# Kernel optimization log

Measured on AMD Instinct MI355X. Metric: run time of the kernel, lower is better.

## Reference

```python
import jax, jax.numpy as jnp
import numpy as np

B, S, HID, NH = 2, 2048, 2048, 16
HD = HID // NH  # head_dim = 128


def setup_inputs() -> dict:
    key = jax.random.key(0)
    ks = jax.random.split(key, 10)
    sc = 1.0 / np.sqrt(HID)
    inp = {
        "hidden_state": jax.random.normal(ks[0], (B, S, HID), dtype=jnp.float32),
        # upper-triangular (strict) causal mask: 1 where attention is forbidden
        "casual_mask": jnp.triu(jnp.ones((S, S), dtype=jnp.float32), k=1),
        # pad last 128 tokens of each sequence
        "pad_mask": jnp.concatenate(
            [jnp.zeros((B, S - 128), jnp.float32), jnp.ones((B, 128), jnp.float32)], axis=1
        ),
        # weights stored [in, out] (transposed vs torch Linear)
        "Wq": jax.random.normal(ks[1], (HID, HID), dtype=jnp.float32) * sc,
        "bq": jnp.zeros((HID,), jnp.float32),
        "Wk": jax.random.normal(ks[2], (HID, HD), dtype=jnp.float32) * sc,
        "bk": jnp.zeros((HD,), jnp.float32),
        "Wv": jax.random.normal(ks[3], (HID, HD), dtype=jnp.float32) * sc,
        "bv": jnp.zeros((HD,), jnp.float32),
        "Wo": jax.random.normal(ks[4], (HID, HID), dtype=jnp.float32) * sc,
        "bo": jnp.zeros((HID,), jnp.float32),
    }
    return inp


def reference(hidden_state, casual_mask, pad_mask, Wq, bq, Wk, bk, Wv, bv, Wo, bo):
    bsz, seq_len, hid = hidden_state.shape
    nh = NH
    hd = hid // nh
    q = hidden_state @ Wq + bq                      # [B,S,HID]
    k = hidden_state @ Wk + bk                      # [B,S,HD]  single shared head
    v = hidden_state @ Wv + bv                      # [B,S,HD]
    q = q.reshape(bsz, seq_len, nh, hd).transpose(0, 2, 1, 3)  # [B,NH,S,HD]
    # attn scores: shared K broadcast across all query heads
    scores = jnp.einsum("bhqd,bkd->bhqk", q, k) / jnp.sqrt(jnp.float32(hd))
    scores = scores + casual_mask * (-1e9)
    scores = scores + pad_mask[:, None, None, :] * (-1e9)
    probs = jax.nn.softmax(scores, axis=-1)         # [B,NH,S,S]
    out = jnp.einsum("bhqk,bkd->bhqd", probs, v)    # [B,NH,S,HD]
    out = out.transpose(0, 2, 1, 3).reshape(bsz, seq_len, hid)
    return out @ Wo + bo
```

## Files before the change

### kernel.cpp

```cpp
#include <hip/hip_runtime.h>
#include <hip/hip_bf16.h>
#include <math.h>

#define B_    2
#define S_    2048
#define HID_  2048
#define NH_   16
#define HD_   128
#define MTOT  4096
#define QKV_N 2304

typedef short bf16x8 __attribute__((ext_vector_type(8)));
typedef float f32x4  __attribute__((ext_vector_type(4)));
typedef float f32x16 __attribute__((ext_vector_type(16)));

__device__ __forceinline__ ushort f2bf(float f) {
    __hip_bfloat16 h = __float2bfloat16(f);
    ushort u; __builtin_memcpy(&u, &h, 2); return u;
}

__device__ __forceinline__ void gload_lds16(const void* g, void* l) {
    __builtin_amdgcn_global_load_lds(
        (const __attribute__((address_space(1))) void*)g,
        (__attribute__((address_space(3))) void*)l, 16, 0, 0);
}
__device__ __forceinline__ void gload_lds4(const void* g, void* l) {
    __builtin_amdgcn_global_load_lds(
        (const __attribute__((address_space(1))) void*)g,
        (__attribute__((address_space(3))) void*)l, 4, 0, 0);
}

__global__ void cast_f32_bf16(const float* __restrict__ in, ushort* __restrict__ out)
{
    long i = ((long)blockIdx.x * 256 + threadIdx.x) * 8;
    float4 a = *(const float4*)&in[i];
    float4 b = *(const float4*)&in[i + 4];
    uint4 o;
    o.x = (uint)f2bf(a.x) | ((uint)f2bf(a.y) << 16);
    o.y = (uint)f2bf(a.z) | ((uint)f2bf(a.w) << 16);
    o.z = (uint)f2bf(b.x) | ((uint)f2bf(b.y) << 16);
    o.w = (uint)f2bf(b.z) | ((uint)f2bf(b.w) << 16);
    *(uint4*)&out[i] = o;
}

__global__ void transcast(const float* __restrict__ W, ushort* __restrict__ T,
                          int N, int rowoff)
{
    __shared__ float tile[32][33];
    const int tx = threadIdx.x & 31, ty = threadIdx.x >> 5;
    const int n0 = blockIdx.x * 32, k0 = blockIdx.y * 32;
#pragma unroll
    for (int i = 0; i < 4; i++)
        tile[ty + 8 * i][tx] = W[(long)(k0 + ty + 8 * i) * N + n0 + tx];
    __syncthreads();
#pragma unroll
    for (int i = 0; i < 4; i++)
        T[(long)(rowoff + n0 + ty + 8 * i) * 2048 + k0 + tx] = f2bf(tile[tx][ty + 8 * i]);
}

__global__ void fuse_bias(const float* __restrict__ bq, const float* __restrict__ bk,
                          const float* __restrict__ bv, float* __restrict__ bqkv)
{
    int i = blockIdx.x * 256 + threadIdx.x;
    if (i < 2048)      bqkv[i] = bq[i];
    else if (i < 2176) bqkv[i] = bk[i - 2048];
    else if (i < QKV_N) bqkv[i] = bv[i - 2176];
}

__global__ __launch_bounds__(256, 2) void gemm_qkv(
    const ushort* __restrict__ A, const ushort* __restrict__ Bt,
    const float* __restrict__ bias,
    ushort* __restrict__ qbuf, ushort* __restrict__ kbuf,
    ushort* __restrict__ vtbuf)
{
    const int K = HID_;
    __shared__ __align__(16) ushort As[128 * 32];
    __shared__ __align__(16) ushort Bs[128 * 32];
    const int t = threadIdx.x;
    const int w = t >> 6, l = t & 63;
    const long bm = (long)blockIdx.y * 128;
    const long bn = (long)blockIdx.x * 128;

    f32x4 acc[4][4];
#pragma unroll
    for (int i = 0; i < 4; i++)
#pragma unroll
        for (int j = 0; j < 4; j++) acc[i][j] = (f32x4){0.f, 0.f, 0.f, 0.f};

    const int srow = w * 16 + (l >> 2);
    const int scol = (l & 3) * 8;
    const ushort* Ag0 = A + (bm + srow) * (long)K + scol;
    const ushort* Ag1 = A + (bm + srow + 64) * (long)K + scol;
    const ushort* Bg0 = Bt + (bn + srow) * (long)K + scol;
    const ushort* Bg1 = Bt + (bn + srow + 64) * (long)K + scol;
    ushort* Al0 = As + w * 512;
    ushort* Al1 = As + 2048 + w * 512;
    ushort* Bl0 = Bs + w * 512;
    ushort* Bl1 = Bs + 2048 + w * 512;

    const int mrow = l & 15, kq = l >> 4;
    const int moff = (w & 1) * 64, noff = (w >> 1) * 64;

    for (int k0 = 0; k0 < K; k0 += 32) {
        gload_lds16(Ag0 + k0, Al0);
        gload_lds16(Ag1 + k0, Al1);
        gload_lds16(Bg0 + k0, Bl0);
        gload_lds16(Bg1 + k0, Bl1);
        __syncthreads();
        bf16x8 af[4], bfr[4];
#pragma unroll
        for (int i = 0; i < 4; i++)
            af[i] = *(const bf16x8*)&As[(moff + i * 16 + mrow) * 32 + kq * 8];
#pragma unroll
        for (int j = 0; j < 4; j++)
            bfr[j] = *(const bf16x8*)&Bs[(noff + j * 16 + mrow) * 32 + kq * 8];
#pragma unroll
        for (int i = 0; i < 4; i++)
#pragma unroll
            for (int j = 0; j < 4; j++)
                acc[i][j] = __builtin_amdgcn_mfma_f32_16x16x32_bf16(
                    af[i], bfr[j], acc[i][j], 0, 0, 0);
        __syncthreads();
    }

    const int crow = (l >> 4) * 4, ccol = l & 15;
    const int tile = blockIdx.x;
#pragma unroll
    for (int i = 0; i < 4; i++) {
#pragma unroll
        for (int j = 0; j < 4; j++) {
            long colg = bn + noff + j * 16 + ccol;
            float bv = bias[colg];
            long row0 = bm + moff + i * 16 + crow;
            float v[4];
#pragma unroll
            for (int r = 0; r < 4; r++) v[r] = acc[i][j][r] + bv;
            if (tile < 16) {
#pragma unroll
                for (int r = 0; r < 4; r++)
                    qbuf[(row0 + r) * (long)HID_ + colg] = f2bf(v[r]);
            } else if (tile == 16) {
                long ck = colg - 2048;
#pragma unroll
                for (int r = 0; r < 4; r++)
                    kbuf[(row0 + r) * (long)HD_ + ck] = f2bf(v[r]);
            } else {
                long cv = colg - 2176;
                long b  = row0 >> 11;
                long s0 = row0 & 2047;
                ushort4 pk;
                pk.x = f2bf(v[0]); pk.y = f2bf(v[1]);
                pk.z = f2bf(v[2]); pk.w = f2bf(v[3]);
                *(ushort4*)&vtbuf[b * (HD_ * (long)S_) + cv * (long)S_ + s0] = pk;
            }
        }
    }
}

__global__ __launch_bounds__(256, 2) void gemm_mfma(
    const ushort* __restrict__ A, const ushort* __restrict__ Bt,
    const float* __restrict__ bias, float* __restrict__ C,
    int K, int ldc)
{
    __shared__ __align__(16) ushort As[128 * 32];
    __shared__ __align__(16) ushort Bs[128 * 32];
    const int t = threadIdx.x;
    const int w = t >> 6, l = t & 63;
    const long bm = (long)blockIdx.y * 128;
    const long bn = (long)blockIdx.x * 128;

    f32x4 acc[4][4];
#pragma unroll
    for (int i = 0; i < 4; i++)
#pragma unroll
        for (int j = 0; j < 4; j++) acc[i][j] = (f32x4){0.f, 0.f, 0.f, 0.f};

    const int srow = w * 16 + (l >> 2);
    const int scol = (l & 3) * 8;
    const ushort* Ag0 = A + (bm + srow) * (long)K + scol;
    const ushort* Ag1 = A + (bm + srow + 64) * (long)K + scol;
    const ushort* Bg0 = Bt + (bn + srow) * (long)K + scol;
    const ushort* Bg1 = Bt + (bn + srow + 64) * (long)K + scol;
    ushort* Al0 = As + w * 512;
    ushort* Al1 = As + 2048 + w * 512;
    ushort* Bl0 = Bs + w * 512;
    ushort* Bl1 = Bs + 2048 + w * 512;

    const int mrow = l & 15, kq = l >> 4;
    const int moff = (w & 1) * 64, noff = (w >> 1) * 64;

    for (int k0 = 0; k0 < K; k0 += 32) {
        gload_lds16(Ag0 + k0, Al0);
        gload_lds16(Ag1 + k0, Al1);
        gload_lds16(Bg0 + k0, Bl0);
        gload_lds16(Bg1 + k0, Bl1);
        __syncthreads();
        bf16x8 af[4], bfr[4];
#pragma unroll
        for (int i = 0; i < 4; i++)
            af[i] = *(const bf16x8*)&As[(moff + i * 16 + mrow) * 32 + kq * 8];
#pragma unroll
        for (int j = 0; j < 4; j++)
            bfr[j] = *(const bf16x8*)&Bs[(noff + j * 16 + mrow) * 32 + kq * 8];
#pragma unroll
        for (int i = 0; i < 4; i++)
#pragma unroll
            for (int j = 0; j < 4; j++)
                acc[i][j] = __builtin_amdgcn_mfma_f32_16x16x32_bf16(
                    af[i], bfr[j], acc[i][j], 0, 0, 0);
        __syncthreads();
    }

    const int crow = (l >> 4) * 4, ccol = l & 15;
#pragma unroll
    for (int i = 0; i < 4; i++) {
#pragma unroll
        for (int j = 0; j < 4; j++) {
            long col = bn + noff + j * 16 + ccol;
            float bv = bias[col];
#pragma unroll
            for (int r = 0; r < 4; r++) {
                long row = bm + moff + i * 16 + crow + r;
                C[row * (long)ldc + col] = acc[i][j][r] + bv;
            }
        }
    }
}

__global__ __launch_bounds__(256, 2) void attn_mfma(
    const ushort* __restrict__ qbuf, const ushort* __restrict__ kbuf,
    const ushort* __restrict__ vtbuf, const float* __restrict__ pad,
    ushort* __restrict__ outp)
{
    __shared__ __align__(16) char smem[34816];
    ushort* Ks   = (ushort*)smem;
    ushort* Vt   = (ushort*)(smem + 16384);
    float*  padL = (float*)(smem + 32768);

    const int qblk = 15 - (int)blockIdx.x;
    const int h = blockIdx.y, b = blockIdx.z;
    const int t = threadIdx.x, w = t >> 6, l = t & 63;
    const int l31 = l & 31, h5 = l >> 5;
    const long rowbase = (long)b * S_;
    const int qbase = qblk * 128 + w * 32;

    bf16x8 qf[8];
    {
        const ushort* qp = qbuf + (rowbase + qbase + l31) * (long)HID_
                                + h * HD_ + h5 * 8;
#pragma unroll
        for (int ks = 0; ks < 8; ks++) qf[ks] = *(const bf16x8*)(qp + ks * 16);
    }

    f32x16 o[4] = {};
    float mrun = -1e30f, lrun = 0.f;

    const ushort* kg[4]; ushort* kl[4];
    const ushort* vg[4]; ushort* vl[4];
#pragma unroll
    for (int i = 0; i < 4; i++) {
        int key0 = w * 16 + i * 4 + (l >> 4);
        int gk = (l & 15) ^ (key0 & 15);
        kg[i] = kbuf + (rowbase + key0) * (long)HD_ + gk * 8;
        kl[i] = Ks + (w * 16 + i * 4) * 128 + l * 8;
        int d = w * 32 + i * 8 + (l >> 3);
        int gv = (l & 7) ^ (d & 7);
        vg[i] = vtbuf + ((long)b * HD_ + d) * (long)S_ + gv * 8;
        vl[i] = Vt + (w * 32 + i * 8) * 64 + l * 8;
    }

    const int kTiles = 2 * qblk + 2;
    const int qmaxw = qbase + 31;
    const float SC  = 0.08838834764831845f * 1.44269504089f;
    const float NEG = -1.0e9f * 1.44269504089f;

    for (int kt = 0; kt < kTiles; kt++) {
        const int ktb = kt * 64;
#pragma unroll
        for (int i = 0; i < 4; i++) gload_lds16(kg[i] + (long)ktb * HD_, kl[i]);
#pragma unroll
        for (int i = 0; i < 4; i++) gload_lds16(vg[i] + ktb, vl[i]);
        if (w == 0) gload_lds4(pad + rowbase + ktb + l, padL);
        __syncthreads();

        if (ktb <= qmaxw) {
            f32x16 c[2] = {};
#pragma unroll
            for (int mb = 0; mb < 2; mb++) {
                const int key = mb * 32 + l31;
#pragma unroll
                for (int ks = 0; ks < 8; ks++) {
                    int g = (ks * 2 + h5) ^ (key & 15);
                    bf16x8 a = *(const bf16x8*)&Ks[key * 128 + g * 8];
                    c[mb] = __builtin_amdgcn_mfma_f32_32x32x16_bf16(
                        a, qf[ks], c[mb], 0, 0, 0);
                }
            }
            const bool causal = (ktb + 63) > qbase;
            const int qg = qbase + l31;
            float vmax = -3.0e38f;
#pragma unroll
            for (int mb = 0; mb < 2; mb++) {
#pragma unroll
                for (int g = 0; g < 4; g++) {
                    float4 pmv = *(const float4*)&padL[mb * 32 + 4 * h5 + 8 * g];
                    float pmr[4] = {pmv.x, pmv.y, pmv.z, pmv.w};
#pragma unroll
                    for (int r = 0; r < 4; r++) {
                        int reg = g * 4 + r;
                        float v = c[mb][reg] * SC + pmr[r] * NEG;
                        if (causal) {
                            int key = ktb + mb * 32 + 4 * h5 + 8 * g + r;
                            if (key > qg) v += NEG;
                        }
                        c[mb][reg] = v;
                        vmax = fmaxf(vmax, v);
                    }
                }
            }
            vmax = fmaxf(vmax, __shfl_xor(vmax, 32));
            float mnew  = fmaxf(mrun, vmax);
            float alpha = __builtin_amdgcn_exp2f(mrun - mnew);
            float sum = 0.f;
#pragma unroll
            for (int mb = 0; mb < 2; mb++)
#pragma unroll
                for (int reg = 0; reg < 16; reg++) {
                    float p = __builtin_amdgcn_exp2f(c[mb][reg] - mnew);
                    c[mb][reg] = p;
                    sum += p;
                }
            sum += __shfl_xor(sum, 32);
            lrun = lrun * alpha + sum;
            mrun = mnew;
#pragma unroll
            for (int mb = 0; mb < 4; mb++) o[mb] *= alpha;

#pragma unroll
            for (int ks2 = 0; ks2 < 4; ks2++) {
                const int mbs = ks2 >> 1;
                const int base = (ks2 & 1) * 8;
                float own[4], oth[4];
#pragma unroll
                for (int i = 0; i < 4; i++) {
                    float ca = c[mbs][base + i];
                    float cb = c[mbs][base + 4 + i];
                    own[i] = h5 ? cb : ca;
                    oth[i] = h5 ? ca : cb;
                }
                float rec[4];
#pragma unroll
                for (int i = 0; i < 4; i++) rec[i] = __shfl_xor(oth[i], 32);
                bf16x8 pf;
#pragma unroll
                for (int i = 0; i < 4; i++) {
                    pf[i]     = (short)f2bf(h5 ? rec[i] : own[i]);
                    pf[4 + i] = (short)f2bf(h5 ? own[i] : rec[i]);
                }
#pragma unroll
                for (int mb = 0; mb < 4; mb++) {
                    int d = mb * 32 + l31;
                    int g = (ks2 * 2 + h5) ^ (d & 7);
                    bf16x8 a = *(const bf16x8*)&Vt[d * 64 + g * 8];
                    o[mb] = __builtin_amdgcn_mfma_f32_32x32x16_bf16(
                        a, pf, o[mb], 0, 0, 0);
                }
            }
        }
        __syncthreads();
    }

    ushort* Ob = (ushort*)smem + w * 4352;
    float inv = 1.f / lrun;
#pragma unroll
    for (int mb = 0; mb < 4; mb++) {
#pragma unroll
        for (int g = 0; g < 4; g++) {
            int d0 = mb * 32 + 4 * h5 + 8 * g;
            ushort4 pk;
            pk.x = f2bf(o[mb][g * 4 + 0] * inv);
            pk.y = f2bf(o[mb][g * 4 + 1] * inv);
            pk.z = f2bf(o[mb][g * 4 + 2] * inv);
            pk.w = f2bf(o[mb][g * 4 + 3] * inv);
            *(ushort4*)&Ob[l31 * 136 + d0] = pk;
        }
    }
    __builtin_amdgcn_s_waitcnt(0);
    {
        const int q = l >> 1, half = l & 1;
        const ushort* src = Ob + q * 136 + half * 64;
        ushort* dst = outp + (rowbase + qblk * 128 + w * 32 + q) * (long)HID_
                           + h * HD_ + half * 64;
#pragma unroll
        for (int i = 0; i < 8; i++) {
            uint4 v = *(const uint4*)(src + i * 8);
            *(uint4*)(dst + i * 8) = v;
        }
    }
}

extern "C" void kernel_launch(void* const* d_in, const int* in_sizes, int n_in,
                              void* d_out, int out_size, void* d_ws, size_t ws_size,
                              hipStream_t stream)
{
    const float* hidden = (const float*)d_in[0];
    const float* pad = (const float*)d_in[2];
    const float* Wq  = (const float*)d_in[3];
    const float* bq  = (const float*)d_in[4];
    const float* Wk  = (const float*)d_in[5];
    const float* bk  = (const float*)d_in[6];
    const float* Wv  = (const float*)d_in[7];
    const float* bv  = (const float*)d_in[8];
    const float* Wo  = (const float*)d_in[9];
    const float* bo  = (const float*)d_in[10];
    float* out = (float*)d_out;

    char* ws = (char*)d_ws;
    ushort* hbf   = (ushort*)(ws);
    ushort* WqkvT = (ushort*)(ws + 16777216);
    ushort* WoT   = (ushort*)(ws + 26214400);
    float*  bqkv  = (float*) (ws + 34603008);
    ushort* qbuf  = (ushort*)(ws + 34619392);
    ushort* kbuf  = (ushort*)(ws + 51396608);
    ushort* vtbuf = (ushort*)(ws + 52445184);
    ushort* attnO = (ushort*)(ws + 53493760);

    cast_f32_bf16<<<4096, 256, 0, stream>>>(hidden, hbf);
    transcast<<<dim3(64, 64), 256, 0, stream>>>(Wq, WqkvT, 2048, 0);
    transcast<<<dim3(4, 64),  256, 0, stream>>>(Wk, WqkvT, 128, 2048);
    transcast<<<dim3(4, 64),  256, 0, stream>>>(Wv, WqkvT, 128, 2176);
    transcast<<<dim3(64, 64), 256, 0, stream>>>(Wo, WoT, 2048, 0);
    fuse_bias<<<9, 256, 0, stream>>>(bq, bk, bv, bqkv);

    gemm_qkv<<<dim3(18, 32), 256, 0, stream>>>(hbf, WqkvT, bqkv,
                                               qbuf, kbuf, vtbuf);
    attn_mfma<<<dim3(16, NH_, B_), 256, 0, stream>>>(qbuf, kbuf, vtbuf, pad,
                                                     attnO);
    gemm_mfma<<<dim3(16, 32), 256, 0, stream>>>(attnO, WoT, bo, out,
                                                HID_, HID_);
}
```

Baseline: 350.8 us.

## Pair causal query blocks per workgroup and double-buffer K/V tiles in LDS

Each attention workgroup now handles two query blocks, one heavy and one light (qblk = 15-x and x), which balances the causal workload, and the grid is halved. The K, V^T and pad tiles are double-buffered in LDS, so the next tile is prefetched while the current one is computed, dropping one barrier per iteration. LDS per block roughly doubles to about 66KB. The grid now yields only one 4-wave block per CU, which reduces concurrent waves available for latency hiding.

```diff
diff --git a/kernel.cpp b/kernel.cpp
--- a/kernel.cpp
+++ b/kernel.cpp
@@ -232,169 +232,192 @@
     const ushort* __restrict__ vtbuf, const float* __restrict__ pad,
     ushort* __restrict__ outp)
 {
-    __shared__ __align__(16) char smem[34816];
-    ushort* Ks   = (ushort*)smem;
-    ushort* Vt   = (ushort*)(smem + 16384);
-    float*  padL = (float*)(smem + 32768);
-
-    const int qblk = 15 - (int)blockIdx.x;
+    __shared__ __align__(16) char smem[66048];
+    ushort* KsB  = (ushort*)smem;
+    ushort* VtB  = (ushort*)(smem + 32768);
+    float*  padB = (float*)(smem + 65536);
+
     const int h = blockIdx.y, b = blockIdx.z;
     const int t = threadIdx.x, w = t >> 6, l = t & 63;
     const int l31 = l & 31, h5 = l >> 5;
     const long rowbase = (long)b * S_;
-    const int qbase = qblk * 128 + w * 32;
-
-    bf16x8 qf[8];
-    {
-        const ushort* qp = qbuf + (rowbase + qbase + l31) * (long)HID_
-                                + h * HD_ + h5 * 8;
-#pragma unroll
-        for (int ks = 0; ks < 8; ks++) qf[ks] = *(const bf16x8*)(qp + ks * 16);
-    }
-
-    f32x16 o[4] = {};
-    float mrun = -1e30f, lrun = 0.f;
-
-    const ushort* kg[4]; ushort* kl[4];
-    const ushort* vg[4]; ushort* vl[4];
+
+    const ushort* kg[4]; int klo[4];
+    const ushort* vg[4]; int vlo[4];
 #pragma unroll
     for (int i = 0; i < 4; i++) {
         int key0 = w * 16 + i * 4 + (l >> 4);
         int gk = (l & 15) ^ (key0 & 15);
         kg[i] = kbuf + (rowbase + key0) * (long)HD_ + gk * 8;
-        kl[i] = Ks + (w * 16 + i * 4) * 128 + l * 8;
+        klo[i] = (w * 16 + i * 4) * 128 + l * 8;
         int d = w * 32 + i * 8 + (l >> 3);
         int gv = (l & 7) ^ (d & 7);
         vg[i] = vtbuf + ((long)b * HD_ + d) * (long)S_ + gv * 8;
-        vl[i] = Vt + (w * 32 + i * 8) * 64 + l * 8;
-    }
-
-    const int kTiles = 2 * qblk + 2;
-    const int qmaxw = qbase + 31;
+        vlo[i] = (w * 32 + i * 8) * 64 + l * 8;
+    }
+
     const float SC  = 0.08838834764831845f * 1.44269504089f;
     const float NEG = -1.0e9f * 1.44269504089f;
 
-    for (int kt = 0; kt < kTiles; kt++) {
-        const int ktb = kt * 64;
-#pragma unroll
-        for (int i = 0; i < 4; i++) gload_lds16(kg[i] + (long)ktb * HD_, kl[i]);
-#pragma unroll
-        for (int i = 0; i < 4; i++) gload_lds16(vg[i] + ktb, vl[i]);
-        if (w == 0) gload_lds4(pad + rowbase + ktb + l, padL);
-        __syncthreads();
-
-        if (ktb <= qmaxw) {
-            f32x16 c[2] = {};
-#pragma unroll
-            for (int mb = 0; mb < 2; mb++) {
-                const int key = mb * 32 + l31;
-#pragma unroll
-                for (int ks = 0; ks < 8; ks++) {
-                    int g = (ks * 2 + h5) ^ (key & 15);
-                    bf16x8 a = *(const bf16x8*)&Ks[key * 128 + g * 8];
-                    c[mb] = __builtin_amdgcn_mfma_f32_32x32x16_bf16(
-                        a, qf[ks], c[mb], 0, 0, 0);
+    for (int pass = 0; pass < 2; ++pass) {
+        const int qblk = pass ? (int)blockIdx.x : 15 - (int)blockIdx.x;
+        const int qbase = qblk * 128 + w * 32;
+        const int kTiles = 2 * qblk + 2;
+        const int qmaxw = qbase + 31;
+
+        bf16x8 qf[8];
+        {
+            const ushort* qp = qbuf + (rowbase + qbase + l31) * (long)HID_
+                                    + h * HD_ + h5 * 8;
+#pragma unroll
+            for (int ks = 0; ks < 8; ks++) qf[ks] = *(const bf16x8*)(qp + ks * 16);
+        }
+
+        f32x16 o[4] = {};
+        float mrun = -1e30f, lrun = 0.f;
+
+        __syncthreads();
+
+#pragma unroll
+        for (int i = 0; i < 4; i++) gload_lds16(kg[i], KsB + klo[i]);
+#pragma unroll
+        for (int i = 0; i < 4; i++) gload_lds16(vg[i], VtB + vlo[i]);
+        if (w == 0) gload_lds4(pad + rowbase + l, padB);
+        __syncthreads();
+
+        for (int kt = 0; kt < kTiles; kt++) {
+            const int cur = kt & 1;
+            const int ktb = kt * 64;
+
+            if (kt + 1 < kTiles) {
+                const int nxt = cur ^ 1;
+                const long nb = (long)(ktb + 64);
+#pragma unroll
+                for (int i = 0; i < 4; i++)
+                    gload_lds16(kg[i] + nb * HD_, KsB + nxt * 8192 + klo[i]);
+#pragma unroll
+                for (int i = 0; i < 4; i++)
+                    gload_lds16(vg[i] + nb, VtB + nxt * 8192 + vlo[i]);
+                if (w == 0) gload_lds4(pad + rowbase + nb + l, padB + nxt * 64);
+            }
+
+            if (ktb <= qmaxw) {
+                const ushort* Ks   = KsB + cur * 8192;
+                const ushort* Vt   = VtB + cur * 8192;
+                const float*  padL = padB + cur * 64;
+
+                f32x16 c[2] = {};
+#pragma unroll
+                for (int mb = 0; mb < 2; mb++) {
+                    const int key = mb * 32 + l31;
+#pragma unroll
+                    for (int ks = 0; ks < 8; ks++) {
+                        int g = (ks * 2 + h5) ^ (key & 15);
+                        bf16x8 a = *(const bf16x8*)&Ks[key * 128 + g * 8];
+                        c[mb] = __builtin_amdgcn_mfma_f32_32x32x16_bf16(
+                            a, qf[ks], c[mb], 0, 0, 0);
+                    }
                 }
-            }
-            const bool causal = (ktb + 63) > qbase;
-            const int qg = qbase + l31;
-            float vmax = -3.0e38f;
-#pragma unroll
-            for (int mb = 0; mb < 2; mb++) {
-#pragma unroll
-                for (int g = 0; g < 4; g++) {
-                    float4 pmv = *(const float4*)&padL[mb * 32 + 4 * h5 + 8 * g];
-                    float pmr[4] = {pmv.x, pmv.y, pmv.z, pmv.w};
-#pragma unroll
-                    for (int r = 0; r < 4; r++) {
-                        int reg = g * 4 + r;
-                        float v = c[mb][reg] * SC + pmr[r] * NEG;
-                        if (causal) {
-                            int key = ktb + mb * 32 + 4 * h5 + 8 * g + r;
-                            if (key > qg) v += NEG;
+                const bool causal = (ktb + 63) > qbase;
+                const int qg = qbase + l31;
+                float vmax = -3.0e38f;
+#pragma unroll
+                for (int mb = 0; mb < 2; mb++) {
+#pragma unroll
+                    for (int g = 0; g < 4; g++) {
+                        float4 pmv = *(const float4*)&padL[mb * 32 + 4 * h5 + 8 * g];
+                        float pmr[4] = {pmv.x, pmv.y, pmv.z, pmv.w};
+#pragma unroll
+                        for (int r = 0; r < 4; r++) {
+                            int reg = g * 4 + r;
+                            float v = c[mb][reg] * SC + pmr[r] * NEG;
+                            if (causal) {
+                                int key = ktb + mb * 32 + 4 * h5 + 8 * g + r;
+                                if (key > qg) v += NEG;
+                            }
+                            c[mb][reg] = v;
+                            vmax = fmaxf(vmax, v);
                         }
-                        c[mb][reg] = v;
-                        vmax = fmaxf(vmax, v);
                     }
                 }
-            }
-            vmax = fmaxf(vmax, __shfl_xor(vmax, 32));
-            float mnew  = fmaxf(mrun, vmax);
-            float alpha = __builtin_amdgcn_exp2f(mrun - mnew);
-            float sum = 0.f;
-#pragma unroll
-            for (int mb = 0; mb < 2; mb++)
-#pragma unroll
-                for (int reg = 0; reg < 16; reg++) {
-                    float p = __builtin_amdgcn_exp2f(c[mb][reg] - mnew);
-                    c[mb][reg] = p;
-                    sum += p;
+                vmax = fmaxf(vmax, __shfl_xor(vmax, 32));
+                float mnew  = fmaxf(mrun, vmax);
+                float alpha = __builtin_amdgcn_exp2f(mrun - mnew);
+                float sum = 0.f;
+#pragma unroll
+                for (int mb = 0; mb < 2; mb++)
+#pragma unroll
+                    for (int reg = 0; reg < 16; reg++) {
+                        float p = __builtin_amdgcn_exp2f(c[mb][reg] - mnew);
+                        c[mb][reg] = p;
+                        sum += p;
+                    }
+                sum += __shfl_xor(sum, 32);
+                lrun = lrun * alpha + sum;
+                mrun = mnew;
+#pragma unroll
+                for (int mb = 0; mb < 4; mb++) o[mb] *= alpha;
+
+#pragma unroll
+                for (int ks2 = 0; ks2 < 4; ks2++) {
+                    const int mbs = ks2 >> 1;
+                    const int base = (ks2 & 1) * 8;
+                    float own[4], oth[4];
+#pragma unroll
+                    for (int i = 0; i < 4; i++) {
+                        float ca = c[mbs][base + i];
+                        float cb = c[mbs][base + 4 + i];
+                        own[i] = h5 ? cb : ca;
+                        oth[i] = h5 ? ca : cb;
+                    }
+                    float rec[4];
+#pragma unroll
+                    for (int i = 0; i < 4; i++) rec[i] = __shfl_xor(oth[i], 32);
+                    bf16x8 pf;
+#pragma unroll
+                    for (int i = 0; i < 4; i++) {
+                        pf[i]     = (short)f2bf(h5 ? rec[i] : own[i]);
+                        pf[4 + i] = (short)f2bf(h5 ? own[i] : rec[i]);
+                    }
+#pragma unroll
+                    for (int mb = 0; mb < 4; mb++) {
+                        int d = mb * 32 + l31;
+                        int g = (ks2 * 2 + h5) ^ (d & 7);
+                        bf16x8 a = *(const bf16x8*)&Vt[d * 64 + g * 8];
+                        o[mb] = __builtin_amdgcn_mfma_f32_32x32x16_bf16(
+                            a, pf, o[mb], 0, 0, 0);
+                    }
                 }
-            sum += __shfl_xor(sum, 32);
-            lrun = lrun * alpha + sum;
-            mrun = mnew;
-#pragma unroll
-            for (int mb = 0; mb < 4; mb++) o[mb] *= alpha;
-
-#pragma unroll
-            for (int ks2 = 0; ks2 < 4; ks2++) {
-                const int mbs = ks2 >> 1;
-                const int base = (ks2 & 1) * 8;
-                float own[4], oth[4];
-#pragma unroll
-                for (int i = 0; i < 4; i++) {
-                    float ca = c[mbs][base + i];
-                    float cb = c[mbs][base + 4 + i];
-                    own[i] = h5 ? cb : ca;
-                    oth[i] = h5 ? ca : cb;
-                }
-                float rec[4];
-#pragma unroll
-                for (int i = 0; i < 4; i++) rec[i] = __shfl_xor(oth[i], 32);
-                bf16x8 pf;
-#pragma unroll
-                for (int i = 0; i < 4; i++) {
-                    pf[i]     = (short)f2bf(h5 ? rec[i] : own[i]);
-                    pf[4 + i] = (short)f2bf(h5 ? own[i] : rec[i]);
-                }
-#pragma unroll
-                for (int mb = 0; mb < 4; mb++) {
-                    int d = mb * 32 + l31;
-                    int g = (ks2 * 2 + h5) ^ (d & 7);
-                    bf16x8 a = *(const bf16x8*)&Vt[d * 64 + g * 8];
-                    o[mb] = __builtin_amdgcn_mfma_f32_32x32x16_bf16(
-                        a, pf, o[mb], 0, 0, 0);
-                }
-            }
-        }
-        __syncthreads();
-    }
-
-    ushort* Ob = (ushort*)smem + w * 4352;
-    float inv = 1.f / lrun;
-#pragma unroll
-    for (int mb = 0; mb < 4; mb++) {
-#pragma unroll
-        for (int g = 0; g < 4; g++) {
-            int d0 = mb * 32 + 4 * h5 + 8 * g;
-            ushort4 pk;
-            pk.x = f2bf(o[mb][g * 4 + 0] * inv);
-            pk.y = f2bf(o[mb][g * 4 + 1] * inv);
-            pk.z = f2bf(o[mb][g * 4 + 2] * inv);
-            pk.w = f2bf(o[mb][g * 4 + 3] * inv);
-            *(ushort4*)&Ob[l31 * 136 + d0] = pk;
-        }
-    }
-    __builtin_amdgcn_s_waitcnt(0);
-    {
-        const int q = l >> 1, half = l & 1;
-        const ushort* src = Ob + q * 136 + half * 64;
-        ushort* dst = outp + (rowbase + qblk * 128 + w * 32 + q) * (long)HID_
-                           + h * HD_ + half * 64;
-#pragma unroll
-        for (int i = 0; i < 8; i++) {
-            uint4 v = *(const uint4*)(src + i * 8);
-            *(uint4*)(dst + i * 8) = v;
+            }
+            __syncthreads();
+        }
+
+        ushort* Ob = (ushort*)smem + w * 4352;
+        float inv = 1.f / lrun;
+#pragma unroll
+        for (int mb = 0; mb < 4; mb++) {
+#pragma unroll
+            for (int g = 0; g < 4; g++) {
+                int d0 = mb * 32 + 4 * h5 + 8 * g;
+                ushort4 pk;
+                pk.x = f2bf(o[mb][g * 4 + 0] * inv);
+                pk.y = f2bf(o[mb][g * 4 + 1] * inv);
+                pk.z = f2bf(o[mb][g * 4 + 2] * inv);
+                pk.w = f2bf(o[mb][g * 4 + 3] * inv);
+                *(ushort4*)&Ob[l31 * 136 + d0] = pk;
+            }
+        }
+        __builtin_amdgcn_s_waitcnt(0);
+        {
+            const int q = l >> 1, half = l & 1;
+            const ushort* src = Ob + q * 136 + half * 64;
+            ushort* dst = outp + (rowbase + qblk * 128 + w * 32 + q) * (long)HID_
+                               + h * HD_ + half * 64;
+#pragma unroll
+            for (int i = 0; i < 8; i++) {
+                uint4 v = *(const uint4*)(src + i * 8);
+                *(uint4*)(dst + i * 8) = v;
+            }
         }
     }
 }
@@ -434,8 +457,8 @@
 
     gemm_qkv<<<dim3(18, 32), 256, 0, stream>>>(hbf, WqkvT, bqkv,
                                                qbuf, kbuf, vtbuf);
-    attn_mfma<<<dim3(16, NH_, B_), 256, 0, stream>>>(qbuf, kbuf, vtbuf, pad,
-                                                     attnO);
+    attn_mfma<<<dim3(8, NH_, B_), 256, 0, stream>>>(qbuf, kbuf, vtbuf, pad,
+                                                    attnO);
     gemm_mfma<<<dim3(16, 32), 256, 0, stream>>>(attnO, WoT, bo, out,
                                                 HID_, HID_);
 }
```

After: 329.5 us. 6.1% less time.
